# Optimization experiments

Measured on AMD Instinct MI355X. Metric: run time of the kernel, lower is better.

The kernel has to match this reference:

```python
import jax, jax.numpy as jnp
import numpy as np
import math

B, P, C, PS = 128, 196, 3, 16      # batch, num_patchs, channels, patch_size
HID, HEADS, HD, FF = 768, 12, 64, 3072
RATE = PS // 4                      # highpass_rate = 4 -> rate = 4
EPS = 1e-5


def _local_highpass(x):
    # x: (B, P, HID) -> per-patch FFT highpass, matching LocalHighPass+HighPass.
    img = x.reshape(B, P, C, PS, PS)
    f = jnp.fft.fftshift(jnp.fft.fft2(img, norm='ortho'), axes=(-2, -1))
    mid = PS // 2
    f = f.at[..., mid - RATE:mid + RATE, mid - RATE:mid + RATE].set(0.0)
    out = jnp.fft.ifft2(jnp.fft.ifftshift(f, axes=(-2, -1)), norm='ortho').real
    return out.reshape(B, P, HID)


def _layernorm(x, g, b):
    m = x.mean(-1, keepdims=True)
    v = ((x - m) ** 2).mean(-1, keepdims=True)
    return (x - m) * jax.lax.rsqrt(v + EPS) * g + b


def setup_inputs() -> dict:
    key = jax.random.key(0)
    ks = jax.random.split(key, 16)
    s_h = 1.0 / math.sqrt(HID)
    s_f = 1.0 / math.sqrt(FF)
    inp = {
        'x': jax.random.normal(ks[0], (B, P, HID), jnp.float32),
        'q_w': jax.random.uniform(ks[1], (HID, HID), jnp.float32, -s_h, s_h),
        'q_b': jnp.zeros((HID,), jnp.float32),
        'k_w': jax.random.uniform(ks[2], (HID, HID), jnp.float32, -s_h, s_h),
        'k_b': jnp.zeros((HID,), jnp.float32),
        'v_w': jax.random.uniform(ks[3], (HID, HID), jnp.float32, -s_h, s_h),
        'v_b': jnp.zeros((HID,), jnp.float32),
        'w1': jax.random.uniform(ks[4], (FF, HID), jnp.float32, -s_h, s_h),
        'b1': jnp.zeros((FF,), jnp.float32),
        'w2': jax.random.uniform(ks[5], (HID, FF), jnp.float32, -s_f, s_f),
        'b2': jnp.zeros((HID,), jnp.float32),
        'ln0_g': jnp.ones((HID,), jnp.float32), 'ln0_b': jnp.zeros((HID,), jnp.float32),
        'ln1_g': jnp.ones((HID,), jnp.float32), 'ln1_b': jnp.zeros((HID,), jnp.float32),
        'ln2_g': jnp.ones((HID,), jnp.float32), 'ln2_b': jnp.zeros((HID,), jnp.float32),
    }
    return inp


def reference(x, q_w, q_b, k_w, k_b, v_w, v_b, w1, b1, w2, b2,
              ln0_g, ln0_b, ln1_g, ln1_b, ln2_g, ln2_b):
    hp = _local_highpass(x)                              # (B, P, HID)
    h = _layernorm(hp, ln0_g, ln0_b)
    # MSAttention (first_block=False, so no position embedding add)
    q = (h @ q_w.T + q_b).reshape(B, P, HEADS, HD)
    k = (h @ k_w.T + k_b).reshape(B, P, HEADS, HD)
    v = (h @ v_w.T + v_b).reshape(B, P, HEADS, HD)
    scores = jnp.einsum('bqhd,bkhd->bhqk', q, k) / math.sqrt(HD)
    probs = jax.nn.softmax(scores, axis=-1)
    ctx = jnp.einsum('bhqk,bkhd->bqhd', probs, v).reshape(B, P, HID)
    h2 = hp + _layernorm(ctx, ln1_g, ln1_b)
    mlp = jax.nn.relu(h2 @ w1.T + b1) @ w2.T + b2
    return h2 + _layernorm(mlp, ln2_g, ln2_b)
```

## Files before the change

kernel.cpp:

```cpp
#include <hip/hip_runtime.h>

#define NTOK   25088
#define HIDD   768
#define NHEAD  12
#define HDIM   64
#define FFD    3072
#define NPAT   196
#define QKVS   2304

typedef __attribute__((ext_vector_type(8))) short short8;
typedef __attribute__((ext_vector_type(8))) __bf16 bf16x8;
typedef __attribute__((ext_vector_type(4))) float f32x4;
typedef __attribute__((ext_vector_type(4))) float fl4;
typedef __attribute__((ext_vector_type(4))) unsigned short us4;
typedef __attribute__((ext_vector_type(8))) unsigned short us8;

#define AS1 __attribute__((address_space(1)))
#define AS3 __attribute__((address_space(3)))

__device__ __forceinline__ unsigned short f2bf(float f) {
  unsigned int u = __builtin_bit_cast(unsigned int, f);
  u += 0x7FFFu + ((u >> 16) & 1u);
  return (unsigned short)(u >> 16);
}
__device__ __forceinline__ float bf2f(unsigned short h) {
  unsigned int u = ((unsigned int)h) << 16;
  return __builtin_bit_cast(float, u);
}

template <typename A>
__device__ __forceinline__ auto mfma_sel(A a, A b, f32x4 c, int)
    -> decltype(__builtin_amdgcn_mfma_f32_16x16x32_bf16(a, b, c, 0, 0, 0)) {
  return __builtin_amdgcn_mfma_f32_16x16x32_bf16(a, b, c, 0, 0, 0);
}
template <typename A>
__device__ __forceinline__ auto mfma_sel(A a, A b, f32x4 c, long)
    -> decltype(__builtin_amdgcn_mfma_f32_16x16x32_bf16(
           __builtin_bit_cast(bf16x8, a), __builtin_bit_cast(bf16x8, b), c, 0, 0, 0)) {
  return __builtin_amdgcn_mfma_f32_16x16x32_bf16(
      __builtin_bit_cast(bf16x8, a), __builtin_bit_cast(bf16x8, b), c, 0, 0, 0);
}
__device__ __forceinline__ f32x4 MFMA16(short8 a, short8 b, f32x4 c) {
  return mfma_sel(a, b, c, 0);
}

__device__ __forceinline__ void gload16(const void* g, void* l) {
  __builtin_amdgcn_global_load_lds((const AS1 void*)g, (AS3 void*)l, 16, 0, 0);
}

__device__ __forceinline__ int swz_bid(int nwg) {
  int orig = (int)blockIdx.x;
  int xcd = orig & 7;
  int q = nwg >> 3, r = nwg & 7;
  int base = (xcd < r) ? xcd * (q + 1) : r * (q + 1) + (xcd - r) * q;
  return base + (orig >> 3);
}

__global__ __launch_bounds__(256) void build_M(unsigned short* __restrict__ Mb) {
  __shared__ float Cs[16], Ss[16];
  int t = threadIdx.x;
  if (t < 16) {
    float c = 0.f;
    for (int k = -4; k <= 3; ++k) c += cosf(0.39269908169872414f * (float)(k * t));
    Cs[t] = c;
    Ss[t] = -sinf(1.5707963267948966f * (float)t);
  }
  __syncthreads();
  int r = t >> 4, cc = t & 15;
  for (int j = 0; j < 256; ++j) {
    int dr = (r - (j >> 4)) & 15;
    int dc = (cc - (j & 15)) & 15;
    float val = ((t == j) ? 1.f : 0.f) - (Cs[dr] * Cs[dc] - Ss[dr] * Ss[dc]) * 0.00390625f;
    Mb[t * 256 + j] = f2bf(val);
  }
}

__global__ __launch_bounds__(256) void castk(const float* __restrict__ s,
                                             unsigned short* __restrict__ d, long n4) {
  for (long i = (long)blockIdx.x * 256 + threadIdx.x; i < n4; i += (long)gridDim.x * 256) {
    fl4 v = *(const fl4*)(s + i * 4);
    us4 o;
    o[0] = f2bf(v[0]); o[1] = f2bf(v[1]); o[2] = f2bf(v[2]); o[3] = f2bf(v[3]);
    *(us4*)(d + i * 4) = o;
  }
}

__global__ __launch_bounds__(256) void bias_cat(const float* __restrict__ qb,
                                                const float* __restrict__ kb,
                                                const float* __restrict__ vb,
                                                float* __restrict__ d) {
  for (int i = threadIdx.x; i < QKVS; i += 256)
    d[i] = (i < 768) ? qb[i] : (i < 1536) ? kb[i - 768] : vb[i - 1536];
}

template <int OUT_BF16, int BIAS, int RELU>
__global__ __launch_bounds__(512, 2) void gemm256(const unsigned short* __restrict__ A,
                                                  const unsigned short* __restrict__ Bm,
                                                  const float* __restrict__ bias,
                                                  void* __restrict__ Cp,
                                                  int Mdim, int Ndim, int Kdim) {
  __shared__ __align__(16) char lds[131072];
  const int nbn = Ndim >> 8;
  const int bid = swz_bid((int)gridDim.x);
  const int bm = bid / nbn, bn = bid % nbn;
  const int t = threadIdx.x;
  const int lane = t & 63, w = t >> 6;
  const int wm = w >> 2, wn = w & 3;
  const int lm = lane & 15, lg = lane >> 4;
  const int NT = Kdim >> 6, NITER = NT >> 1;

  const int tr = t >> 3;
  const int scol = ((t & 7) ^ (tr & 7)) * 8;
  const unsigned short* Asrc = A + (size_t)(bm * 256 + tr) * Kdim + scol;
  const unsigned short* Bsrc = Bm + (size_t)(bn * 256 + tr) * Kdim + scol;
  const size_t K64 = (size_t)64 * Kdim, K128 = (size_t)128 * Kdim, K192 = (size_t)192 * Kdim;

  char* const d0 = lds;
  char* const d1 = lds + 65536;

  auto SA = [&](int kt, int d) {
    char* dst = lds + d * 65536;
    const unsigned short* s = Asrc + kt * 64;
    gload16(s, dst + t * 16);
    gload16(s + K64, dst + 8192 + t * 16);
    gload16(s + K128, dst + 16384 + t * 16);
    gload16(s + K192, dst + 24576 + t * 16);
  };
  auto SB = [&](int kt, int d, int h) {
    char* dst = lds + d * 65536 + 32768 + h * 16384;
    const unsigned short* s = Bsrc + kt * 64 + (h ? K128 : 0);
    gload16(s, dst + t * 16);
    gload16(s + K64, dst + 8192 + t * 16);
  };

  const int sx = lm & 7;
  int slotb[2];
#pragma unroll
  for (int kk = 0; kk < 2; ++kk) slotb[kk] = (((kk << 2) | lg) ^ sx) << 4;
  const int aoff = wm * 16384 + lm * 128;
  const int boff = 32768 + (wn >> 1) * 16384 + ((wn & 1) * 64 + lm) * 128;

  f32x4 acc[8][4];
#pragma unroll
  for (int i = 0; i < 8; ++i)
#pragma unroll
    for (int j = 0; j < 4; ++j) acc[i][j] = (f32x4){0.f, 0.f, 0.f, 0.f};
  short8 bqA[4][2], bqB[4][2];

  auto RDB = [&](const char* db, short8 (&bq)[4][2]) {
#pragma unroll
    for (int ni = 0; ni < 4; ++ni)
#pragma unroll
      for (int kk = 0; kk < 2; ++kk)
        bq[ni][kk] = *(const short8*)(db + boff + ni * 2048 + slotb[kk]);
  };
  auto PH = [&](const char* db, int q, short8 (&bq)[4][2], int vmc) {
    short8 aq[2][2];
#pragma unroll
    for (int m2 = 0; m2 < 2; ++m2)
#pragma unroll
      for (int kk = 0; kk < 2; ++kk)
        aq[m2][kk] = *(const short8*)(db + aoff + q * 4096 + m2 * 2048 + slotb[kk]);
    __builtin_amdgcn_s_barrier();
    asm volatile("s_waitcnt lgkmcnt(0)" ::: "memory");
    __builtin_amdgcn_sched_barrier(0);
    __builtin_amdgcn_s_setprio(1);
#pragma unroll
    for (int kk = 0; kk < 2; ++kk)
#pragma unroll
      for (int m2 = 0; m2 < 2; ++m2)
#pragma unroll
        for (int ni = 0; ni < 4; ++ni)
          acc[q * 2 + m2][ni] = MFMA16(aq[m2][kk], bq[ni][kk], acc[q * 2 + m2][ni]);
    __builtin_amdgcn_s_setprio(0);
    if (vmc == 8)      asm volatile("s_waitcnt vmcnt(8)" ::: "memory");
    else if (vmc == 4) asm volatile("s_waitcnt vmcnt(4)" ::: "memory");
    else if (vmc == 0) asm volatile("s_waitcnt vmcnt(0)" ::: "memory");
    __builtin_amdgcn_s_barrier();
    __builtin_amdgcn_sched_barrier(0);
  };

  SA(0, 0); SB(0, 0, 0); SB(0, 0, 1); SB(1, 1, 0); SB(1, 1, 1);
  asm volatile("s_waitcnt vmcnt(4)" ::: "memory");
  __builtin_amdgcn_s_barrier();
  __builtin_amdgcn_sched_barrier(0);
  RDB(d0, bqA);

  for (int j = 0; j < NITER; ++j) {
    const bool nl = (j + 1 < NITER);
    const int t2 = 2 * j + 2, t3 = 2 * j + 3;
    SA(2 * j + 1, 1);       PH(d0, 0, bqA, -1);
    if (nl) SB(t2, 0, 0);   PH(d0, 1, bqA, -1);
    if (nl) SB(t2, 0, 1);   PH(d0, 2, bqA, nl ? 8 : 4);
    RDB(d1, bqB);           PH(d0, 3, bqA, nl ? 4 : 0);
    if (nl) SA(t2, 0);      PH(d1, 0, bqB, -1);
    if (nl) SB(t3, 1, 0);   PH(d1, 1, bqB, -1);
    if (nl) SB(t3, 1, 1);   PH(d1, 2, bqB, nl ? 8 : -1);
    if (nl) RDB(d0, bqA);   PH(d1, 3, bqB, nl ? 4 : -1);
  }

  const int row0 = bm * 256 + wm * 128 + lg * 4;
  const int col0 = bn * 256 + wn * 64 + lm;
#pragma unroll
  for (int mi = 0; mi < 8; ++mi) {
#pragma unroll
    for (int ni = 0; ni < 4; ++ni) {
      int col = col0 + ni * 16;
      float bia = BIAS ? bias[col] : 0.f;
#pragma unroll
      for (int rg = 0; rg < 4; ++rg) {
        int row = row0 + mi * 16 + rg;
        float vv = acc[mi][ni][rg] + bia;
        if (RELU) vv = vv > 0.f ? vv : 0.f;
        if (OUT_BF16)
          ((unsigned short*)Cp)[(size_t)row * Ndim + col] = f2bf(vv);
        else
          ((float*)Cp)[(size_t)row * Ndim + col] = vv;
      }
    }
  }
}

template <int OUT_BF16, int BIAS, int RELU>
__global__ __launch_bounds__(512, 4) void gemm128(const unsigned short* __restrict__ A,
                                                  const unsigned short* __restrict__ Bm,
                                                  const float* __restrict__ bias,
                                                  void* __restrict__ Cp,
                                                  int Mdim, int Ndim, int Kdim) {
  __shared__ __align__(16) char lds[65536];
  const int nbn = Ndim >> 7;
  const int bid = swz_bid((int)gridDim.x);
  const int bm = bid / nbn, bn = bid % nbn;
  const int t = threadIdx.x;
  const int lane = t & 63, w = t >> 6;
  const int wm = w >> 2, wn = w & 3;
  const int lm = lane & 15, lg = lane >> 4;
  const int NITER = Kdim >> 7;

  const int tr = t >> 3;
  const int scol = ((t & 7) ^ (tr & 7)) * 8;
  const unsigned short* Asrc = A + (size_t)(bm * 128 + tr) * Kdim + scol;
  const unsigned short* Bsrc = Bm + (size_t)(bn * 128 + tr) * Kdim + scol;
  const size_t K64 = (size_t)64 * Kdim;

  char* const d0 = lds;
  char* const d1 = lds + 32768;

  auto SA = [&](int kt, int d) {
    char* dst = lds + d * 32768;
    const unsigned short* s = Asrc + kt * 64;
    gload16(s, dst + t * 16);
    gload16(s + K64, dst + 8192 + t * 16);
  };
  auto SB = [&](int kt, int d, int h) {
    char* dst = lds + d * 32768 + 16384 + h * 8192;
    gload16(Bsrc + kt * 64 + (h ? K64 : 0), dst + t * 16);
  };

  const int sx = lm & 7;
  int slotb[2];
#pragma unroll
  for (int kk = 0; kk < 2; ++kk) slotb[kk] = (((kk << 2) | lg) ^ sx) << 4;
  const int aoff = (wm * 64 + lm) * 128;
  const int boff = 16384 + (wn * 32 + lm) * 128;

  f32x4 acc[4][2];
#pragma unroll
  for (int i = 0; i < 4; ++i)
#pragma unroll
    for (int j = 0; j < 2; ++j) acc[i][j] = (f32x4){0.f, 0.f, 0.f, 0.f};
  short8 bqA[2][2], bqB[2][2];

  auto RDB = [&](const char* db, short8 (&bq)[2][2]) {
#pragma unroll
    for (int ni = 0; ni < 2; ++ni)
#pragma unroll
      for (int kk = 0; kk < 2; ++kk)
        bq[ni][kk] = *(const short8*)(db + boff + ni * 2048 + slotb[kk]);
  };
  auto PH = [&](const char* db, int q, short8 (&bq)[2][2], int vmc) {
    short8 aq[2];
#pragma unroll
    for (int kk = 0; kk < 2; ++kk)
      aq[kk] = *(const short8*)(db + aoff + q * 2048 + slotb[kk]);
    __builtin_amdgcn_s_barrier();
    asm volatile("s_waitcnt lgkmcnt(0)" ::: "memory");
    __builtin_amdgcn_sched_barrier(0);
    __builtin_amdgcn_s_setprio(1);
#pragma unroll
    for (int kk = 0; kk < 2; ++kk)
#pragma unroll
      for (int ni = 0; ni < 2; ++ni)
        acc[q][ni] = MFMA16(aq[kk], bq[ni][kk], acc[q][ni]);
    __builtin_amdgcn_s_setprio(0);
    if (vmc == 4)      asm volatile("s_waitcnt vmcnt(4)" ::: "memory");
    else if (vmc == 2) asm volatile("s_waitcnt vmcnt(2)" ::: "memory");
    else if (vmc == 0) asm volatile("s_waitcnt vmcnt(0)" ::: "memory");
    __builtin_amdgcn_s_barrier();
    __builtin_amdgcn_sched_barrier(0);
  };

  SA(0, 0); SB(0, 0, 0); SB(0, 0, 1); SB(1, 1, 0); SB(1, 1, 1);
  asm volatile("s_waitcnt vmcnt(2)" ::: "memory");
  __builtin_amdgcn_s_barrier();
  __builtin_amdgcn_sched_barrier(0);
  RDB(d0, bqA);

  for (int j = 0; j < NITER; ++j) {
    const bool nl = (j + 1 < NITER);
    const int t2 = 2 * j + 2, t3 = 2 * j + 3;
    SA(2 * j + 1, 1);       PH(d0, 0, bqA, -1);
    if (nl) SB(t2, 0, 0);   PH(d0, 1, bqA, -1);
    if (nl) SB(t2, 0, 1);   PH(d0, 2, bqA, nl ? 4 : 2);
    RDB(d1, bqB);           PH(d0, 3, bqA, nl ? 2 : 0);
    if (nl) SA(t2, 0);      PH(d1, 0, bqB, -1);
    if (nl) SB(t3, 1, 0);   PH(d1, 1, bqB, -1);
    if (nl) SB(t3, 1, 1);   PH(d1, 2, bqB, nl ? 4 : -1);
    if (nl) RDB(d0, bqA);   PH(d1, 3, bqB, nl ? 2 : -1);
  }

  const int row0 = bm * 128 + wm * 64 + lg * 4;
  const int col0 = bn * 128 + wn * 32 + lm;
#pragma unroll
  for (int mi = 0; mi < 4; ++mi) {
#pragma unroll
    for (int ni = 0; ni < 2; ++ni) {
      int col = col0 + ni * 16;
      float bia = BIAS ? bias[col] : 0.f;
#pragma unroll
      for (int rg = 0; rg < 4; ++rg) {
        int row = row0 + mi * 16 + rg;
        float vv = acc[mi][ni][rg] + bia;
        if (RELU) vv = vv > 0.f ? vv : 0.f;
        if (OUT_BF16)
          ((unsigned short*)Cp)[(size_t)row * Ndim + col] = f2bf(vv);
        else
          ((float*)Cp)[(size_t)row * Ndim + col] = vv;
      }
    }
  }
}

__global__ __launch_bounds__(256) void ln0_k(const unsigned short* __restrict__ x,
                                             const float* __restrict__ g,
                                             const float* __restrict__ bb,
                                             unsigned short* __restrict__ out) {
  int w = threadIdx.x >> 6, lane = threadIdx.x & 63;
  long row = (long)blockIdx.x * 4 + w;
  const unsigned short* xr = x + row * HIDD;
  float xv[12];
  float s1 = 0.f, s2 = 0.f;
#pragma unroll
  for (int c = 0; c < 3; ++c) {
    us4 u = *(const us4*)(xr + c * 256 + lane * 4);
#pragma unroll
    for (int j = 0; j < 4; ++j) {
      float f = bf2f(u[j]);
      xv[c * 4 + j] = f; s1 += f; s2 += f * f;
    }
  }
#pragma unroll
  for (int off = 32; off; off >>= 1) { s1 += __shfl_xor(s1, off); s2 += __shfl_xor(s2, off); }
  float m = s1 * (1.f / 768.f);
  float rs = rsqrtf(s2 * (1.f / 768.f) - m * m + 1e-5f);
#pragma unroll
  for (int c = 0; c < 3; ++c) {
    int cb = c * 256 + lane * 4;
    us4 o;
#pragma unroll
    for (int j = 0; j < 4; ++j) o[j] = f2bf((xv[c * 4 + j] - m) * rs * g[cb + j] + bb[cb + j]);
    *(us4*)(out + row * HIDD + cb) = o;
  }
}

__global__ __launch_bounds__(256) void ln1_k(const unsigned short* __restrict__ ctx,
                                             const unsigned short* __restrict__ hp,
                                             const float* __restrict__ g,
                                             const float* __restrict__ bb,
                                             unsigned short* __restrict__ h2b) {
  int w = threadIdx.x >> 6, lane = threadIdx.x & 63;
  long row = (long)blockIdx.x * 4 + w;
  const unsigned short* xr = ctx + row * HIDD;
  float xv[12];
  float s1 = 0.f, s2 = 0.f;
#pragma unroll
  for (int c = 0; c < 3; ++c) {
    us4 u = *(const us4*)(xr + c * 256 + lane * 4);
#pragma unroll
    for (int j = 0; j < 4; ++j) {
      float f = bf2f(u[j]);
      xv[c * 4 + j] = f; s1 += f; s2 += f * f;
    }
  }
#pragma unroll
  for (int off = 32; off; off >>= 1) { s1 += __shfl_xor(s1, off); s2 += __shfl_xor(s2, off); }
  float m = s1 * (1.f / 768.f);
  float rs = rsqrtf(s2 * (1.f / 768.f) - m * m + 1e-5f);
#pragma unroll
  for (int c = 0; c < 3; ++c) {
    int cb = c * 256 + lane * 4;
    us4 hv = *(const us4*)(hp + row * HIDD + cb);
    us4 ob;
#pragma unroll
    for (int j = 0; j < 4; ++j)
      ob[j] = f2bf(bf2f(hv[j]) + (xv[c * 4 + j] - m) * rs * g[cb + j] + bb[cb + j]);
    *(us4*)(h2b + row * HIDD + cb) = ob;
  }
}

__global__ __launch_bounds__(256) void ln2_k(float* __restrict__ mlp2_out,
                                             const unsigned short* __restrict__ h2b,
                                             const float* __restrict__ g,
                                             const float* __restrict__ bb) {
  int w = threadIdx.x >> 6, lane = threadIdx.x & 63;
  long row = (long)blockIdx.x * 4 + w;
  float* xr = mlp2_out + row * HIDD;
  fl4 v[3];
  float s1 = 0.f, s2 = 0.f;
#pragma unroll
  for (int c = 0; c < 3; ++c) {
    v[c] = *(const fl4*)(xr + c * 256 + lane * 4);
#pragma unroll
    for (int j = 0; j < 4; ++j) { s1 += v[c][j]; s2 += v[c][j] * v[c][j]; }
  }
#pragma unroll
  for (int off = 32; off; off >>= 1) { s1 += __shfl_xor(s1, off); s2 += __shfl_xor(s2, off); }
  float m = s1 * (1.f / 768.f);
  float rs = rsqrtf(s2 * (1.f / 768.f) - m * m + 1e-5f);
#pragma unroll
  for (int c = 0; c < 3; ++c) {
    int cb = c * 256 + lane * 4;
    us4 hv = *(const us4*)(h2b + row * HIDD + cb);
    fl4 o;
#pragma unroll
    for (int j = 0; j < 4; ++j)
      o[j] = bf2f(hv[j]) + (v[c][j] - m) * rs * g[cb + j] + bb[cb + j];
    *(fl4*)(xr + cb) = o;
  }
}

__global__ __launch_bounds__(256, 2) void attn_k(const unsigned short* __restrict__ qkv,
                                                 unsigned short* __restrict__ ctx) {
  __shared__ __align__(16) unsigned short Ks[NPAT * 64];
  __shared__ __align__(16) unsigned short VT[64 * 232];
  __shared__ __align__(16) unsigned short PL[4][16 * 40];
  const int b = blockIdx.x / NHEAD, h = blockIdx.x % NHEAD;
  const int t = threadIdx.x, lane = t & 63, w = t >> 6;
  const size_t base = ((size_t)b * NPAT) * QKVS + h * HDIM;

  for (int idx = t; idx < NPAT * 8; idx += 256) {
    int row = idx >> 3, s = idx & 7;
    us8 kv = *(const us8*)&qkv[base + 768 + (size_t)row * QKVS + s * 8];
    *(us8*)((char*)Ks + row * 128 + ((s ^ (row & 7)) << 4)) = kv;
  }
  for (int idx = t; idx < 98 * 64; idx += 256) {
    int pp = idx >> 6, d = idx & 63;
    unsigned int val = (unsigned int)qkv[base + 1536 + (size_t)(2 * pp) * QKVS + d]
                     | ((unsigned int)qkv[base + 1536 + (size_t)(2 * pp + 1) * QKVS + d] << 16);
    *(unsigned int*)&VT[d * 232 + 2 * pp] = val;
  }
  for (int idx = t; idx < 64 * 18; idx += 256) {
    int d = idx / 18, c = idx % 18;
    *(unsigned int*)&VT[d * 232 + 196 + 2 * c] = 0;
  }
  __syncthreads();

  unsigned short* plw = (unsigned short*)PL[w];
  const int lm = lane & 15, lg = lane >> 4, lk = lg * 8;

  for (int qt = w; qt < 13; qt += 4) {
    const int q0 = qt * 16;
    int qrow = q0 + lm; if (qrow > NPAT - 1) qrow = NPAT - 1;
    short8 af0 = *(const short8*)&qkv[base + (size_t)qrow * QKVS + lk];
    short8 af1 = *(const short8*)&qkv[base + (size_t)qrow * QKVS + 32 + lk];

    f32x4 sc[13];
#pragma unroll
    for (int kt = 0; kt < 13; ++kt) {
      int krow = kt * 16 + lm; if (krow > NPAT - 1) krow = NPAT - 1;
      const char* krp = (const char*)Ks + krow * 128;
      short8 b0 = *(const short8*)(krp + (((lg ^ (krow & 7)) & 7) << 4));
      short8 b1 = *(const short8*)(krp + ((((lg + 4) ^ (krow & 7)) & 7) << 4));
      f32x4 z = (f32x4){0.f, 0.f, 0.f, 0.f};
      z = MFMA16(af0, b0, z);
      sc[kt] = MFMA16(af1, b1, z);
    }
#pragma unroll
    for (int kt = 0; kt < 13; ++kt) {
      int col = kt * 16 + lm;
#pragma unroll
      for (int rg = 0; rg < 4; ++rg) {
        float s = sc[kt][rg] * 0.125f;
        sc[kt][rg] = (col < NPAT) ? s : -1e30f;
      }
    }
    float inv[4];
#pragma unroll
    for (int rg = 0; rg < 4; ++rg) {
      float m = -1e30f;
#pragma unroll
      for (int kt = 0; kt < 13; ++kt) m = fmaxf(m, sc[kt][rg]);
      m = fmaxf(m, __shfl_xor(m, 1)); m = fmaxf(m, __shfl_xor(m, 2));
      m = fmaxf(m, __shfl_xor(m, 4)); m = fmaxf(m, __shfl_xor(m, 8));
      float s = 0.f;
#pragma unroll
      for (int kt = 0; kt < 13; ++kt) { float e = __expf(sc[kt][rg] - m); sc[kt][rg] = e; s += e; }
      s += __shfl_xor(s, 1); s += __shfl_xor(s, 2); s += __shfl_xor(s, 4); s += __shfl_xor(s, 8);
      inv[rg] = 1.f / s;
    }

    f32x4 oacc[4];
#pragma unroll
    for (int ni = 0; ni < 4; ++ni) oacc[ni] = (f32x4){0.f, 0.f, 0.f, 0.f};
#pragma unroll
    for (int kc = 0; kc < 7; ++kc) {
#pragma unroll
      for (int sub = 0; sub < 2; ++sub) {
        const int kt = 2 * kc + sub;
#pragma unroll
        for (int rg = 0; rg < 4; ++rg) {
          unsigned short pv_ = 0;
          if (kt < 13) pv_ = f2bf(sc[kt][rg] * inv[rg]);
          plw[(lg * 4 + rg) * 40 + sub * 16 + lm] = pv_;
        }
      }
      asm volatile("s_waitcnt lgkmcnt(0)" ::: "memory");
      __builtin_amdgcn_sched_barrier(0);
      short8 pa = *(const short8*)&plw[lm * 40 + lk];
#pragma unroll
      for (int ni = 0; ni < 4; ++ni) {
        short8 bv = *(const short8*)&VT[(ni * 16 + lm) * 232 + kc * 32 + lk];
        oacc[ni] = MFMA16(pa, bv, oacc[ni]);
      }
    }
#pragma unroll
    for (int rg = 0; rg < 4; ++rg) {
      int r = q0 + lg * 4 + rg;
      if (r < NPAT) {
#pragma unroll
        for (int ni = 0; ni < 4; ++ni)
          ctx[((size_t)b * NPAT + r) * HIDD + h * HDIM + ni * 16 + lm] = f2bf(oacc[ni][rg]);
      }
    }
  }
}

extern "C" void kernel_launch(void* const* d_in, const int* in_sizes, int n_in,
                              void* d_out, int out_size, void* d_ws, size_t ws_size,
                              hipStream_t stream) {
  const float* x    = (const float*)d_in[0];
  const float* q_w  = (const float*)d_in[1];
  const float* q_b  = (const float*)d_in[2];
  const float* k_w  = (const float*)d_in[3];
  const float* k_b  = (const float*)d_in[4];
  const float* v_w  = (const float*)d_in[5];
  const float* v_b  = (const float*)d_in[6];
  const float* w1   = (const float*)d_in[7];
  const float* b1   = (const float*)d_in[8];
  const float* w2   = (const float*)d_in[9];
  const float* b2   = (const float*)d_in[10];
  const float* ln0g = (const float*)d_in[11];
  const float* ln0b = (const float*)d_in[12];
  const float* ln1g = (const float*)d_in[13];
  const float* ln1b = (const float*)d_in[14];
  const float* ln2g = (const float*)d_in[15];
  const float* ln2b = (const float*)d_in[16];

  char* ws = (char*)d_ws;
  size_t o = 0;
  auto alloc = [&](size_t bytes) { size_t r = o; o += (bytes + 255) & ~(size_t)255; return r; };

  const size_t RSZ = (size_t)NTOK * HIDD * 2;
  unsigned short* Mb    = (unsigned short*)(ws + alloc(256 * 256 * 2));
  unsigned short* wqkvb = (unsigned short*)(ws + alloc((size_t)QKVS * HIDD * 2));
  unsigned short* w1b   = (unsigned short*)(ws + alloc((size_t)FFD * HIDD * 2));
  unsigned short* w2b   = (unsigned short*)(ws + alloc((size_t)HIDD * FFD * 2));
  float*          qkvbias = (float*)(ws + alloc(QKVS * 4));
  char* rA  = ws + alloc(RSZ);
  char* rB  = ws + alloc(RSZ);
  char* rC0 = ws + alloc(RSZ);
  char* rC1 = ws + alloc(RSZ);
  char* rC2 = ws + alloc(RSZ);
  char* rC3 = ws + alloc(RSZ);
  (void)rC2; (void)rC3; (void)n_in; (void)in_sizes; (void)ws_size;

  unsigned short* xb  = (unsigned short*)rC0;
  unsigned short* hpb = (unsigned short*)rA;
  unsigned short* hb  = (unsigned short*)rB;
  unsigned short* qkv = (unsigned short*)rC1;
  unsigned short* cxb = (unsigned short*)rC0;
  unsigned short* h2b = (unsigned short*)rB;
  unsigned short* m1b = (unsigned short*)rC0;
  float*          m2f = (float*)d_out;

  build_M<<<1, 256, 0, stream>>>(Mb);
  bias_cat<<<1, 256, 0, stream>>>(q_b, k_b, v_b, qkvbias);

  auto cgrid = [](long n4) { long g = (n4 + 255) / 256; return (int)(g > 2048 ? 2048 : g); };
  long nx4 = (long)NTOK * HIDD / 4;
  castk<<<cgrid(nx4), 256, 0, stream>>>(x, xb, nx4);
  long nw4 = (long)HIDD * HIDD / 4;
  castk<<<cgrid(nw4), 256, 0, stream>>>(q_w, wqkvb, nw4);
  castk<<<cgrid(nw4), 256, 0, stream>>>(k_w, wqkvb + (size_t)768 * HIDD, nw4);
  castk<<<cgrid(nw4), 256, 0, stream>>>(v_w, wqkvb + (size_t)1536 * HIDD, nw4);
  long nf4 = (long)FFD * HIDD / 4;
  castk<<<cgrid(nf4), 256, 0, stream>>>(w1, w1b, nf4);
  castk<<<cgrid(nf4), 256, 0, stream>>>(w2, w2b, nf4);

  gemm128<1, 0, 0><<<588 * 2, 512, 0, stream>>>(xb, Mb, nullptr, hpb, 75264, 256, 256);
  ln0_k<<<NTOK / 4, 256, 0, stream>>>(hpb, ln0g, ln0b, hb);

  gemm256<1, 1, 0><<<98 * 9, 512, 0, stream>>>(hb, wqkvb, qkvbias, qkv, NTOK, QKVS, HIDD);

  attn_k<<<128 * NHEAD, 256, 0, stream>>>(qkv, cxb);

  ln1_k<<<NTOK / 4, 256, 0, stream>>>(cxb, hpb, ln1g, ln1b, h2b);

  gemm256<1, 1, 1><<<98 * 12, 512, 0, stream>>>(h2b, w1b, b1, m1b, NTOK, FFD, HIDD);
  gemm128<0, 1, 0><<<196 * 6, 512, 0, stream>>>(m1b, w2b, b2, m2f, NTOK, HIDD, FFD);

  ln2_k<<<NTOK / 4, 256, 0, stream>>>(m2f, h2b, ln2g, ln2b);
  (void)out_size;
}
```

Measured before the change: 599.6 us.

## Merge GEMM main-loop phases into two larger MFMA phases per tile

Restructures the 256x256 GEMM mainloop from four phases per K-tile into two. Each phase now loads A fragments for two quarter-blocks and issues 32 MFMAs. B-tile staging is merged into one call that issues four loads, and the vmcnt waits are adjusted to match. This halves the number of barriers and waitcnt sync points per K-tile. In exchange, more A-fragment registers are live and global loads interleave with compute at a coarser grain. The RDB of the next buffer now runs earlier, so the vmcnt accounting must still guarantee that data has landed before it is read.

```diff
diff --git a/kernel.cpp b/kernel.cpp
--- a/kernel.cpp
+++ b/kernel.cpp
@@ -126,11 +126,13 @@
     gload16(s + K128, dst + 16384 + t * 16);
     gload16(s + K192, dst + 24576 + t * 16);
   };
-  auto SB = [&](int kt, int d, int h) {
-    char* dst = lds + d * 65536 + 32768 + h * 16384;
-    const unsigned short* s = Bsrc + kt * 64 + (h ? K128 : 0);
+  auto SB = [&](int kt, int d) {
+    char* dst = lds + d * 65536 + 32768;
+    const unsigned short* s = Bsrc + kt * 64;
     gload16(s, dst + t * 16);
     gload16(s + K64, dst + 8192 + t * 16);
+    gload16(s + K128, dst + 16384 + t * 16);
+    gload16(s + K192, dst + 24576 + t * 16);
   };
 
   const int sx = lm & 7;
@@ -154,13 +156,16 @@
       for (int kk = 0; kk < 2; ++kk)
         bq[ni][kk] = *(const short8*)(db + boff + ni * 2048 + slotb[kk]);
   };
-  auto PH = [&](const char* db, int q, short8 (&bq)[4][2], int vmc) {
-    short8 aq[2][2];
-#pragma unroll
-    for (int m2 = 0; m2 < 2; ++m2)
-#pragma unroll
-      for (int kk = 0; kk < 2; ++kk)
-        aq[m2][kk] = *(const short8*)(db + aoff + q * 4096 + m2 * 2048 + slotb[kk]);
+  auto PH2 = [&](const char* db, int qp, short8 (&bq)[4][2], int vmc) {
+    short8 aq[2][2][2];
+#pragma unroll
+    for (int ql = 0; ql < 2; ++ql)
+#pragma unroll
+      for (int m2 = 0; m2 < 2; ++m2)
+#pragma unroll
+        for (int kk = 0; kk < 2; ++kk)
+          aq[ql][m2][kk] =
+              *(const short8*)(db + aoff + (qp * 2 + ql) * 4096 + m2 * 2048 + slotb[kk]);
     __builtin_amdgcn_s_barrier();
     asm volatile("s_waitcnt lgkmcnt(0)" ::: "memory");
     __builtin_amdgcn_sched_barrier(0);
@@ -168,19 +173,21 @@
 #pragma unroll
     for (int kk = 0; kk < 2; ++kk)
 #pragma unroll
-      for (int m2 = 0; m2 < 2; ++m2)
-#pragma unroll
-        for (int ni = 0; ni < 4; ++ni)
-          acc[q * 2 + m2][ni] = MFMA16(aq[m2][kk], bq[ni][kk], acc[q * 2 + m2][ni]);
+      for (int ql = 0; ql < 2; ++ql)
+#pragma unroll
+        for (int m2 = 0; m2 < 2; ++m2)
+#pragma unroll
+          for (int ni = 0; ni < 4; ++ni)
+            acc[(qp * 2 + ql) * 2 + m2][ni] =
+                MFMA16(aq[ql][m2][kk], bq[ni][kk], acc[(qp * 2 + ql) * 2 + m2][ni]);
     __builtin_amdgcn_s_setprio(0);
-    if (vmc == 8)      asm volatile("s_waitcnt vmcnt(8)" ::: "memory");
-    else if (vmc == 4) asm volatile("s_waitcnt vmcnt(4)" ::: "memory");
+    if (vmc == 4)      asm volatile("s_waitcnt vmcnt(4)" ::: "memory");
     else if (vmc == 0) asm volatile("s_waitcnt vmcnt(0)" ::: "memory");
     __builtin_amdgcn_s_barrier();
     __builtin_amdgcn_sched_barrier(0);
   };
 
-  SA(0, 0); SB(0, 0, 0); SB(0, 0, 1); SB(1, 1, 0); SB(1, 1, 1);
+  SA(0, 0); SB(0, 0); SB(1, 1);
   asm volatile("s_waitcnt vmcnt(4)" ::: "memory");
   __builtin_amdgcn_s_barrier();
   __builtin_amdgcn_sched_barrier(0);
@@ -188,15 +195,11 @@
 
   for (int j = 0; j < NITER; ++j) {
     const bool nl = (j + 1 < NITER);
-    const int t2 = 2 * j + 2, t3 = 2 * j + 3;
-    SA(2 * j + 1, 1);       PH(d0, 0, bqA, -1);
-    if (nl) SB(t2, 0, 0);   PH(d0, 1, bqA, -1);
-    if (nl) SB(t2, 0, 1);   PH(d0, 2, bqA, nl ? 8 : 4);
-    RDB(d1, bqB);           PH(d0, 3, bqA, nl ? 4 : 0);
-    if (nl) SA(t2, 0);      PH(d1, 0, bqB, -1);
-    if (nl) SB(t3, 1, 0);   PH(d1, 1, bqB, -1);
-    if (nl) SB(t3, 1, 1);   PH(d1, 2, bqB, nl ? 8 : -1);
-    if (nl) RDB(d0, bqA);   PH(d1, 3, bqB, nl ? 4 : -1);
+    const int t1 = 2 * j + 1, t2 = 2 * j + 2, t3 = 2 * j + 3;
+    SA(t1, 1);                            PH2(d0, 0, bqA, 4);
+    if (nl) SB(t2, 0);  RDB(d1, bqB);     PH2(d0, 1, bqA, nl ? 4 : 0);
+    if (nl) SA(t2, 0);                    PH2(d1, 0, bqB, nl ? 4 : -1);
+    if (nl) { SB(t3, 1); RDB(d0, bqA); }  PH2(d1, 1, bqB, nl ? 4 : -1);
   }
 
   const int row0 = bm * 256 + wm * 128 + lg * 4;
```

New measurement: 922.1 us. 1.54x slower.

## Restructure GEMM pipeline to triple-buffer A tiles with single B buffer

Applied to the files above, without the earlier changes.

Replaces the two-stage double-buffered A/B LDS layout with three rotating A buffers plus a single B buffer, issuing B loads one tile ahead and A loads two tiles ahead. The main loop is unrolled by six tiles so the A-buffer rotation and B-fragment register ping-pong stay compile-time static. The aim is to prefetch A further ahead and hide global-load latency better within the same 128KB of LDS. It requires K/64 to be divisible by 6 (768 and 3072 both qualify) and relies on the B register prefetch being read before the shared B buffer is overwritten.

```diff
diff --git a/kernel.cpp b/kernel.cpp
--- a/kernel.cpp
+++ b/kernel.cpp
@@ -107,7 +107,7 @@
   const int lane = t & 63, w = t >> 6;
   const int wm = w >> 2, wn = w & 3;
   const int lm = lane & 15, lg = lane >> 4;
-  const int NT = Kdim >> 6, NITER = NT >> 1;
+  const int NT = Kdim >> 6;
 
   const int tr = t >> 3;
   const int scol = ((t & 7) ^ (tr & 7)) * 8;
@@ -115,22 +115,24 @@
   const unsigned short* Bsrc = Bm + (size_t)(bn * 256 + tr) * Kdim + scol;
   const size_t K64 = (size_t)64 * Kdim, K128 = (size_t)128 * Kdim, K192 = (size_t)192 * Kdim;
 
-  char* const d0 = lds;
-  char* const d1 = lds + 65536;
-
-  auto SA = [&](int kt, int d) {
-    char* dst = lds + d * 65536;
+  char* const A0 = lds;
+  char* const A1 = lds + 32768;
+  char* const A2 = lds + 65536;
+  char* const Bb = lds + 98304;
+
+  auto SA = [&](int kt, char* abuf) {
     const unsigned short* s = Asrc + kt * 64;
-    gload16(s, dst + t * 16);
-    gload16(s + K64, dst + 8192 + t * 16);
-    gload16(s + K128, dst + 16384 + t * 16);
-    gload16(s + K192, dst + 24576 + t * 16);
-  };
-  auto SB = [&](int kt, int d, int h) {
-    char* dst = lds + d * 65536 + 32768 + h * 16384;
-    const unsigned short* s = Bsrc + kt * 64 + (h ? K128 : 0);
-    gload16(s, dst + t * 16);
-    gload16(s + K64, dst + 8192 + t * 16);
+    gload16(s, abuf + t * 16);
+    gload16(s + K64, abuf + 8192 + t * 16);
+    gload16(s + K128, abuf + 16384 + t * 16);
+    gload16(s + K192, abuf + 24576 + t * 16);
+  };
+  auto SB = [&](int kt) {
+    const unsigned short* s = Bsrc + kt * 64;
+    gload16(s, Bb + t * 16);
+    gload16(s + K64, Bb + 8192 + t * 16);
+    gload16(s + K128, Bb + 16384 + t * 16);
+    gload16(s + K192, Bb + 24576 + t * 16);
   };
 
   const int sx = lm & 7;
@@ -138,7 +140,7 @@
 #pragma unroll
   for (int kk = 0; kk < 2; ++kk) slotb[kk] = (((kk << 2) | lg) ^ sx) << 4;
   const int aoff = wm * 16384 + lm * 128;
-  const int boff = 32768 + (wn >> 1) * 16384 + ((wn & 1) * 64 + lm) * 128;
+  const int boff = (wn >> 1) * 16384 + ((wn & 1) * 64 + lm) * 128;
 
   f32x4 acc[8][4];
 #pragma unroll
@@ -147,20 +149,20 @@
     for (int j = 0; j < 4; ++j) acc[i][j] = (f32x4){0.f, 0.f, 0.f, 0.f};
   short8 bqA[4][2], bqB[4][2];
 
-  auto RDB = [&](const char* db, short8 (&bq)[4][2]) {
+  auto RDB = [&](short8 (&bq)[4][2]) {
 #pragma unroll
     for (int ni = 0; ni < 4; ++ni)
 #pragma unroll
       for (int kk = 0; kk < 2; ++kk)
-        bq[ni][kk] = *(const short8*)(db + boff + ni * 2048 + slotb[kk]);
-  };
-  auto PH = [&](const char* db, int q, short8 (&bq)[4][2], int vmc) {
+        bq[ni][kk] = *(const short8*)(Bb + boff + ni * 2048 + slotb[kk]);
+  };
+  auto PH = [&](const char* abuf, int q, short8 (&bq)[4][2], int vmc) {
     short8 aq[2][2];
 #pragma unroll
     for (int m2 = 0; m2 < 2; ++m2)
 #pragma unroll
       for (int kk = 0; kk < 2; ++kk)
-        aq[m2][kk] = *(const short8*)(db + aoff + q * 4096 + m2 * 2048 + slotb[kk]);
+        aq[m2][kk] = *(const short8*)(abuf + aoff + q * 4096 + m2 * 2048 + slotb[kk]);
     __builtin_amdgcn_s_barrier();
     asm volatile("s_waitcnt lgkmcnt(0)" ::: "memory");
     __builtin_amdgcn_sched_barrier(0);
@@ -173,30 +175,41 @@
         for (int ni = 0; ni < 4; ++ni)
           acc[q * 2 + m2][ni] = MFMA16(aq[m2][kk], bq[ni][kk], acc[q * 2 + m2][ni]);
     __builtin_amdgcn_s_setprio(0);
-    if (vmc == 8)      asm volatile("s_waitcnt vmcnt(8)" ::: "memory");
-    else if (vmc == 4) asm volatile("s_waitcnt vmcnt(4)" ::: "memory");
+    if (vmc == 4)      asm volatile("s_waitcnt vmcnt(4)" ::: "memory");
     else if (vmc == 0) asm volatile("s_waitcnt vmcnt(0)" ::: "memory");
     __builtin_amdgcn_s_barrier();
     __builtin_amdgcn_sched_barrier(0);
   };
 
-  SA(0, 0); SB(0, 0, 0); SB(0, 0, 1); SB(1, 1, 0); SB(1, 1, 1);
+  auto TILE = [&](int i, char* curA, char* nxtA, short8 (&cur)[4][2], short8 (&nxt)[4][2]) {
+    const bool h1 = (i + 1 < NT), h2 = (i + 2 < NT);
+    if (h1) SB(i + 1);
+    if (h2) SA(i + 2, nxtA);
+    PH(curA, 0, cur, -1);
+    PH(curA, 1, cur, -1);
+    PH(curA, 2, cur, h2 ? 4 : (h1 ? 0 : -1));
+    if (h1) RDB(nxt);
+    PH(curA, 3, cur, -1);
+  };
+
+  SA(0, A0); SB(0); SA(1, A1);
   asm volatile("s_waitcnt vmcnt(4)" ::: "memory");
   __builtin_amdgcn_s_barrier();
   __builtin_amdgcn_sched_barrier(0);
-  RDB(d0, bqA);
-
-  for (int j = 0; j < NITER; ++j) {
-    const bool nl = (j + 1 < NITER);
-    const int t2 = 2 * j + 2, t3 = 2 * j + 3;
-    SA(2 * j + 1, 1);       PH(d0, 0, bqA, -1);
-    if (nl) SB(t2, 0, 0);   PH(d0, 1, bqA, -1);
-    if (nl) SB(t2, 0, 1);   PH(d0, 2, bqA, nl ? 8 : 4);
-    RDB(d1, bqB);           PH(d0, 3, bqA, nl ? 4 : 0);
-    if (nl) SA(t2, 0);      PH(d1, 0, bqB, -1);
-    if (nl) SB(t3, 1, 0);   PH(d1, 1, bqB, -1);
-    if (nl) SB(t3, 1, 1);   PH(d1, 2, bqB, nl ? 8 : -1);
-    if (nl) RDB(d0, bqA);   PH(d1, 3, bqB, nl ? 4 : -1);
+  RDB(bqA);
+  asm volatile("s_waitcnt lgkmcnt(0)" ::: "memory");
+  __builtin_amdgcn_sched_barrier(0);
+  __builtin_amdgcn_s_barrier();
+  __builtin_amdgcn_sched_barrier(0);
+
+  for (int J = 0; J < NT / 6; ++J) {
+    const int b6 = J * 6;
+    TILE(b6 + 0, A0, A2, bqA, bqB);
+    TILE(b6 + 1, A1, A0, bqB, bqA);
+    TILE(b6 + 2, A2, A1, bqA, bqB);
+    TILE(b6 + 3, A0, A2, bqB, bqA);
+    TILE(b6 + 4, A1, A0, bqA, bqB);
+    TILE(b6 + 5, A2, A1, bqB, bqA);
   }
 
   const int row0 = bm * 256 + wm * 128 + lg * 4;
```

Result: no change. 594.3 us (-0.9%).
